# Kernel optimization log

Measured on AMD Instinct MI355X. Metric: run time of the kernel, lower is better.

Reference implementation:

```python
import jax, jax.numpy as jnp
import numpy as np

# cv2 GrabCut label codes
GC_BGD, GC_FGD, GC_PR_BGD, GC_PR_FGD = 0, 1, 2, 3
ITER_COUNT = 5
GAMMA = 50.0  # smoothness weight (GrabCut's standard gamma)

B, C, H, W = 2, 256, 512, 512


def setup_inputs() -> dict:
    key = jax.random.key(0)
    k1, k2 = jax.random.split(key)
    features = jax.random.normal(k1, (B, C, H, W), dtype=jnp.float32)
    mask = jax.random.randint(k2, (B, H, W), 0, 2, dtype=jnp.int32)
    return {"features": features, "mask": mask}


def _neighbor_mean(a):
    # a: (B,H,W); 4-neighbor mean with edge replication (smoothness/pairwise term)
    p = jnp.pad(a, ((0, 0), (1, 1), (1, 1)), mode="edge")
    return (p[:, :-2, 1:-1] + p[:, 2:, 1:-1] + p[:, 1:-1, :-2] + p[:, 1:-1, 2:]) * 0.25


def reference(features, mask):
    b, c, h, w = features.shape
    # take first 3 channels as pseudo-RGB image, HWC layout
    img = jnp.transpose(features[:, :3], (0, 2, 3, 1))  # (B,H,W,3)
    # cv2.normalize(..., 0, 255, NORM_MINMAX) over the whole array, then uint8 cast
    mn = img.min(axis=(1, 2, 3), keepdims=True)
    mx = img.max(axis=(1, 2, 3), keepdims=True)
    img = jnp.clip(jnp.floor((img - mn) / (mx - mn + 1e-12) * 255.0), 0.0, 255.0)

    # trimap seeding exactly as in the torch module
    tri = jnp.where(mask == 1, GC_PR_FGD, GC_PR_BGD).astype(jnp.int32)
    bh, bw = int(h * 0.1), int(w * 0.1)
    tri = tri.at[:, :bh, :].set(GC_BGD)
    tri = tri.at[:, h - bh:, :].set(GC_BGD)
    tri = tri.at[:, :, :bw].set(GC_BGD)
    tri = tri.at[:, :, w - bw:].set(GC_BGD)
    tri = tri.at[:, int(h * 0.45):int(h * 0.55), int(w * 0.45):int(w * 0.55)].set(GC_FGD)

    fixed = (tri == GC_BGD) | (tri == GC_FGD)          # hard constraints never change
    fixed_fg = (tri == GC_FGD).astype(img.dtype)
    alpha = ((tri == GC_FGD) | (tri == GC_PR_FGD)).astype(img.dtype)  # fg indicator

    # GrabCut surrogate: iteratively (1) refit fg/bg color models from current
    # labeling (GMM step collapsed to per-region mean), (2) relabel probable
    # pixels by unary (color distance) + pairwise (neighbor agreement) energy
    # -- an ICM approximation of the min-cut step.
    for _ in range(ITER_COUNT):
        a4 = alpha[..., None]                                    # (B,H,W,1)
        fg_mean = (img * a4).sum((1, 2)) / (a4.sum((1, 2)) + 1e-6)        # (B,3)
        bg_mean = (img * (1.0 - a4)).sum((1, 2)) / ((1.0 - a4).sum((1, 2)) + 1e-6)
        d_fg = ((img - fg_mean[:, None, None, :]) ** 2).sum(-1)  # (B,H,W)
        d_bg = ((img - bg_mean[:, None, None, :]) ** 2).sum(-1)
        nb = _neighbor_mean(alpha)
        score = d_bg - d_fg + GAMMA * (2.0 * nb - 1.0)           # >0 -> foreground
        new_alpha = (score > 0).astype(img.dtype)
        alpha = jnp.where(fixed, fixed_fg, new_alpha)

    return alpha  # (B,H,W) in {0,1}, float32
```

## Files before the change

kernel.cpp:

```cpp
#include <hip/hip_runtime.h>
#include <stdint.h>
#include <stddef.h>

#pragma clang fp contract(off)

#define HH 512
#define WW 512
#define HW_ 262144
#define FEAT_BSTRIDE (256*HW_)

__device__ __forceinline__ float quantf(float f, float mn, float denom) {
  float v = (f - mn) / denom * 255.0f;
  v = floorf(v);
  return fminf(fmaxf(v, 0.0f), 255.0f);
}

__device__ __forceinline__ bool is_center(int y, int x) {
  return (y >= 230) & (y < 281) & (x >= 230) & (x < 281);
}
__device__ __forceinline__ bool is_border(int y, int x) {
  return (y < 51) | (y >= 461) | (x < 51) | (x >= 461);
}

__global__ __launch_bounds__(256) void k_minmax(const float* __restrict__ feat,
                                                float2* __restrict__ mm) {
  int blk = blockIdx.x, tid = threadIdx.x;
  int b = blk >> 7, ib = blk & 127;
  const float4* base =
      reinterpret_cast<const float4*>(feat + (size_t)b * FEAT_BSTRIDE) + (size_t)ib * 1536;
  float mn = 3.4e38f, mx = -3.4e38f;
#pragma unroll
  for (int j = 0; j < 6; j++) {
    float4 v = base[tid + j * 256];
    mn = fminf(mn, fminf(fminf(v.x, v.y), fminf(v.z, v.w)));
    mx = fmaxf(mx, fmaxf(fmaxf(v.x, v.y), fmaxf(v.z, v.w)));
  }
  __shared__ float smn[256], smx[256];
  smn[tid] = mn; smx[tid] = mx;
  __syncthreads();
  for (int s = 128; s >= 1; s >>= 1) {
    if (tid < s) {
      smn[tid] = fminf(smn[tid], smn[tid + s]);
      smx[tid] = fmaxf(smx[tid], smx[tid + s]);
    }
    __syncthreads();
  }
  if (tid == 0) mm[blk] = make_float2(smn[0], smx[0]);
}

__global__ __launch_bounds__(256) void k_init(const float* __restrict__ feat,
                                              const int* __restrict__ mask,
                                              const float2* __restrict__ mm,
                                              uint8_t* __restrict__ alphaA,
                                              int4* __restrict__ totals,
                                              int4* __restrict__ slot0) {
  int blk = blockIdx.x, tid = threadIdx.x;
  int b = blk >> 7;
  __shared__ float smn[128], smx[128];
  if (tid < 128) { float2 v = mm[b * 128 + tid]; smn[tid] = v.x; smx[tid] = v.y; }
  __syncthreads();
  for (int s = 64; s >= 1; s >>= 1) {
    if (tid < s) {
      smn[tid] = fminf(smn[tid], smn[tid + s]);
      smx[tid] = fmaxf(smx[tid], smx[tid + s]);
    }
    __syncthreads();
  }
  float mn = smn[0];
  float denom = (smx[0] - mn) + 1e-12f;
  const float* fb = feat + (size_t)b * FEAT_BSTRIDE;
  int a0 = 0, a1 = 0, a2 = 0, a3 = 0, t0 = 0, t1 = 0, t2 = 0;
#pragma unroll
  for (int j = 0; j < 8; j++) {
    int p = blk * 2048 + tid + j * 256;
    int pb = p & (HW_ - 1);
    int y = pb >> 9, x = pb & 511;
    int r  = (int)quantf(fb[pb], mn, denom);
    int g  = (int)quantf(fb[HW_ + pb], mn, denom);
    int bl = (int)quantf(fb[2 * HW_ + pb], mn, denom);
    int a;
    if (is_center(y, x)) a = 1;
    else if (is_border(y, x)) a = 0;
    else a = (mask[p] == 1) ? 1 : 0;
    alphaA[p] = (uint8_t)a;
    a0 += r * a; a1 += g * a; a2 += bl * a; a3 += a;
    t0 += r; t1 += g; t2 += bl;
  }
  __shared__ int red[256][8];
  red[tid][0] = a0; red[tid][1] = a1; red[tid][2] = a2; red[tid][3] = a3;
  red[tid][4] = t0; red[tid][5] = t1; red[tid][6] = t2; red[tid][7] = 0;
  __syncthreads();
  for (int s = 128; s >= 1; s >>= 1) {
    if (tid < s) {
#pragma unroll
      for (int j = 0; j < 7; j++) red[tid][j] += red[tid + s][j];
    }
    __syncthreads();
  }
  if (tid == 0) {
    slot0[blk]  = make_int4(red[0][0], red[0][1], red[0][2], red[0][3]);
    totals[blk] = make_int4(red[0][4], red[0][5], red[0][6], 0);
  }
}

__global__ __launch_bounds__(256) void k_relabel(const float* __restrict__ feat,
                                                 const uint8_t* __restrict__ ain,
                                                 uint8_t* __restrict__ aout,
                                                 const float2* __restrict__ mm,
                                                 const int4* __restrict__ totals,
                                                 const int4* __restrict__ slotIn,
                                                 int4* __restrict__ slotOut,
                                                 float* __restrict__ out,
                                                 int finalIter) {
  int blk = blockIdx.x, tid = threadIdx.x;
  int b = blk >> 7;
  __shared__ float smn[128], smx[128];
  __shared__ int red[128][8];
  if (tid < 128) {
    float2 v = mm[b * 128 + tid]; smn[tid] = v.x; smx[tid] = v.y;
    int4 s = slotIn[b * 128 + tid];
    int4 t = totals[b * 128 + tid];
    red[tid][0] = s.x; red[tid][1] = s.y; red[tid][2] = s.z; red[tid][3] = s.w;
    red[tid][4] = t.x; red[tid][5] = t.y; red[tid][6] = t.z; red[tid][7] = 0;
  }
  __syncthreads();
  for (int s = 64; s >= 1; s >>= 1) {
    if (tid < s) {
      smn[tid] = fminf(smn[tid], smn[tid + s]);
      smx[tid] = fmaxf(smx[tid], smx[tid + s]);
#pragma unroll
      for (int j = 0; j < 7; j++) red[tid][j] += red[tid + s][j];
    }
    __syncthreads();
  }
  __shared__ float fmv[3], bmv[3];
  if (tid == 0) {
    int cnt = red[0][3];
    float fden = (float)cnt + 1e-6f;
    float bden = (float)(HW_ - cnt) + 1e-6f;
#pragma unroll
    for (int c = 0; c < 3; c++) {
      fmv[c] = (float)red[0][c] / fden;
      bmv[c] = (float)(red[0][4 + c] - red[0][c]) / bden;
    }
  }
  __syncthreads();
  float f0 = fmv[0], f1 = fmv[1], f2 = fmv[2];
  float g0 = bmv[0], g1 = bmv[1], g2 = bmv[2];
  float mn = smn[0];
  float denom = (smx[0] - smn[0]) + 1e-12f;
  const float* fb = feat + (size_t)b * FEAT_BSTRIDE;
  int a0 = 0, a1 = 0, a2 = 0, a3 = 0;
#pragma unroll
  for (int j = 0; j < 8; j++) {
    int p = blk * 2048 + tid + j * 256;
    int pb = p & (HW_ - 1);
    int y = pb >> 9, x = pb & 511;
    float i0 = quantf(fb[pb], mn, denom);
    float i1 = quantf(fb[HW_ + pb], mn, denom);
    float i2 = quantf(fb[2 * HW_ + pb], mn, denom);
    int up = ain[p - (y > 0 ? WW : 0)];
    int dn = ain[p + (y < HH - 1 ? WW : 0)];
    int lf = ain[p - (x > 0 ? 1 : 0)];
    int rt = ain[p + (x < WW - 1 ? 1 : 0)];
    float nb = (float)(((up + dn) + lf) + rt) * 0.25f;
    float pair = 50.0f * ((2.0f * nb) - 1.0f);
    float t0 = i0 - f0, t1 = i1 - f1, t2 = i2 - f2;
    float df = ((t0 * t0) + (t1 * t1)) + (t2 * t2);
    float u0 = i0 - g0, u1 = i1 - g1, u2 = i2 - g2;
    float db = ((u0 * u0) + (u1 * u1)) + (u2 * u2);
    float score = (db - df) + pair;
    int a;
    if (is_center(y, x)) a = 1;
    else if (is_border(y, x)) a = 0;
    else a = (score > 0.0f) ? 1 : 0;
    aout[p] = (uint8_t)a;
    if (finalIter) out[p] = (float)a;
    int ri = (int)i0, gi = (int)i1, bi = (int)i2;
    a0 += ri * a; a1 += gi * a; a2 += bi * a; a3 += a;
  }
  __shared__ int red2[256][4];
  red2[tid][0] = a0; red2[tid][1] = a1; red2[tid][2] = a2; red2[tid][3] = a3;
  __syncthreads();
  for (int s = 128; s >= 1; s >>= 1) {
    if (tid < s) {
#pragma unroll
      for (int j = 0; j < 4; j++) red2[tid][j] += red2[tid + s][j];
    }
    __syncthreads();
  }
  if (tid == 0) slotOut[blk] = make_int4(red2[0][0], red2[0][1], red2[0][2], red2[0][3]);
}

extern "C" void kernel_launch(void* const* d_in, const int* in_sizes, int n_in,
                              void* d_out, int out_size, void* d_ws, size_t ws_size,
                              hipStream_t stream) {
  const float* feat = (const float*)d_in[0];
  const int*   mask = (const int*)d_in[1];
  float* out = (float*)d_out;

  char* ws = (char*)d_ws;
  uint8_t* aA     = (uint8_t*)(ws);
  uint8_t* aB     = (uint8_t*)(ws + 524288);
  float2*  mm     = (float2*)(ws + 1048576);
  int4*    totals = (int4*)(ws + 1050624);
  int4*    slots  = (int4*)(ws + 1054720);

  k_minmax<<<256, 256, 0, stream>>>(feat, mm);
  k_init<<<256, 256, 0, stream>>>(feat, mask, mm, aA, totals, slots );

  uint8_t* ain = aA;
  uint8_t* aout_buf = aB;
  for (int k = 0; k < 5; k++) {
    k_relabel<<<256, 256, 0, stream>>>(feat, ain, aout_buf, mm, totals,
                                       slots + (size_t)k * 256,
                                       slots + (size_t)(k + 1) * 256,
                                       out, (k == 4) ? 1 : 0);
    uint8_t* tmp = ain; ain = aout_buf; aout_buf = tmp;
  }
}
```

Measured before the change: 626.7 us.

## Fuse minmax, init and relabel iterations into one cooperative kernel

Replaces seven separate kernel launches with one cooperative kernel that uses grid-wide syncs between phases. Each thread keeps its raw and then quantized RGB values in registers, so the feature channels are read from global memory once instead of in every phase. This removes launch overhead and the repeated feature reads. In exchange it adds grid.sync barriers and more register pressure, and it relies on all 256 blocks being co-resident.

```diff
diff --git a/kernel.cpp b/kernel.cpp
--- a/kernel.cpp
+++ b/kernel.cpp
@@ -1,8 +1,11 @@
 #include <hip/hip_runtime.h>
+#include <hip/hip_cooperative_groups.h>
 #include <stdint.h>
 #include <stddef.h>
 
 #pragma clang fp contract(off)
+
+namespace cg = cooperative_groups;
 
 #define HH 512
 #define WW 512
@@ -22,20 +25,32 @@
   return (y < 51) | (y >= 461) | (x < 51) | (x >= 461);
 }
 
-__global__ __launch_bounds__(256) void k_minmax(const float* __restrict__ feat,
-                                                float2* __restrict__ mm) {
-  int blk = blockIdx.x, tid = threadIdx.x;
-  int b = blk >> 7, ib = blk & 127;
-  const float4* base =
-      reinterpret_cast<const float4*>(feat + (size_t)b * FEAT_BSTRIDE) + (size_t)ib * 1536;
+__global__ __launch_bounds__(256) void k_fused(
+    const float* __restrict__ feat, const int* __restrict__ mask,
+    uint8_t* __restrict__ aA, uint8_t* __restrict__ aB,
+    float2* __restrict__ mm, int4* __restrict__ totals,
+    int4* __restrict__ slots, float* __restrict__ out)
+{
+  cg::grid_group grid = cg::this_grid();
+  const int blk = blockIdx.x, tid = threadIdx.x;
+  const int b = blk >> 7;
+  const float* fb = feat + (size_t)b * FEAT_BSTRIDE;
+  const int pbase = blk * 2048 + tid;
+
+  __shared__ float smn[256], smx[256];
+  __shared__ int red[256][8];
+  __shared__ float fmv[3], bmv[3];
+
+  float rq[8], gq[8], bq[8];
   float mn = 3.4e38f, mx = -3.4e38f;
 #pragma unroll
-  for (int j = 0; j < 6; j++) {
-    float4 v = base[tid + j * 256];
-    mn = fminf(mn, fminf(fminf(v.x, v.y), fminf(v.z, v.w)));
-    mx = fmaxf(mx, fmaxf(fmaxf(v.x, v.y), fmaxf(v.z, v.w)));
-  }
-  __shared__ float smn[256], smx[256];
+  for (int j = 0; j < 8; j++) {
+    int pb = (pbase + j * 256) & (HW_ - 1);
+    float r = fb[pb], g = fb[HW_ + pb], bl = fb[2 * HW_ + pb];
+    rq[j] = r; gq[j] = g; bq[j] = bl;
+    mn = fminf(mn, fminf(fminf(r, g), bl));
+    mx = fmaxf(mx, fmaxf(fmaxf(r, g), bl));
+  }
   smn[tid] = mn; smx[tid] = mx;
   __syncthreads();
   for (int s = 128; s >= 1; s >>= 1) {
@@ -46,17 +61,8 @@
     __syncthreads();
   }
   if (tid == 0) mm[blk] = make_float2(smn[0], smx[0]);
-}
-
-__global__ __launch_bounds__(256) void k_init(const float* __restrict__ feat,
-                                              const int* __restrict__ mask,
-                                              const float2* __restrict__ mm,
-                                              uint8_t* __restrict__ alphaA,
-                                              int4* __restrict__ totals,
-                                              int4* __restrict__ slot0) {
-  int blk = blockIdx.x, tid = threadIdx.x;
-  int b = blk >> 7;
-  __shared__ float smn[128], smx[128];
+  grid.sync();
+
   if (tid < 128) { float2 v = mm[b * 128 + tid]; smn[tid] = v.x; smx[tid] = v.y; }
   __syncthreads();
   for (int s = 64; s >= 1; s >>= 1) {
@@ -66,130 +72,123 @@
     }
     __syncthreads();
   }
-  float mn = smn[0];
-  float denom = (smx[0] - mn) + 1e-12f;
-  const float* fb = feat + (size_t)b * FEAT_BSTRIDE;
-  int a0 = 0, a1 = 0, a2 = 0, a3 = 0, t0 = 0, t1 = 0, t2 = 0;
+  mn = smn[0];
+  const float denom = (smx[0] - mn) + 1e-12f;
+
 #pragma unroll
   for (int j = 0; j < 8; j++) {
-    int p = blk * 2048 + tid + j * 256;
-    int pb = p & (HW_ - 1);
-    int y = pb >> 9, x = pb & 511;
-    int r  = (int)quantf(fb[pb], mn, denom);
-    int g  = (int)quantf(fb[HW_ + pb], mn, denom);
-    int bl = (int)quantf(fb[2 * HW_ + pb], mn, denom);
-    int a;
-    if (is_center(y, x)) a = 1;
-    else if (is_border(y, x)) a = 0;
-    else a = (mask[p] == 1) ? 1 : 0;
-    alphaA[p] = (uint8_t)a;
-    a0 += r * a; a1 += g * a; a2 += bl * a; a3 += a;
-    t0 += r; t1 += g; t2 += bl;
-  }
-  __shared__ int red[256][8];
-  red[tid][0] = a0; red[tid][1] = a1; red[tid][2] = a2; red[tid][3] = a3;
-  red[tid][4] = t0; red[tid][5] = t1; red[tid][6] = t2; red[tid][7] = 0;
-  __syncthreads();
-  for (int s = 128; s >= 1; s >>= 1) {
-    if (tid < s) {
-#pragma unroll
-      for (int j = 0; j < 7; j++) red[tid][j] += red[tid + s][j];
-    }
-    __syncthreads();
-  }
-  if (tid == 0) {
-    slot0[blk]  = make_int4(red[0][0], red[0][1], red[0][2], red[0][3]);
-    totals[blk] = make_int4(red[0][4], red[0][5], red[0][6], 0);
-  }
-}
-
-__global__ __launch_bounds__(256) void k_relabel(const float* __restrict__ feat,
-                                                 const uint8_t* __restrict__ ain,
-                                                 uint8_t* __restrict__ aout,
-                                                 const float2* __restrict__ mm,
-                                                 const int4* __restrict__ totals,
-                                                 const int4* __restrict__ slotIn,
-                                                 int4* __restrict__ slotOut,
-                                                 float* __restrict__ out,
-                                                 int finalIter) {
-  int blk = blockIdx.x, tid = threadIdx.x;
-  int b = blk >> 7;
-  __shared__ float smn[128], smx[128];
-  __shared__ int red[128][8];
-  if (tid < 128) {
-    float2 v = mm[b * 128 + tid]; smn[tid] = v.x; smx[tid] = v.y;
-    int4 s = slotIn[b * 128 + tid];
-    int4 t = totals[b * 128 + tid];
-    red[tid][0] = s.x; red[tid][1] = s.y; red[tid][2] = s.z; red[tid][3] = s.w;
-    red[tid][4] = t.x; red[tid][5] = t.y; red[tid][6] = t.z; red[tid][7] = 0;
-  }
-  __syncthreads();
-  for (int s = 64; s >= 1; s >>= 1) {
-    if (tid < s) {
-      smn[tid] = fminf(smn[tid], smn[tid + s]);
-      smx[tid] = fmaxf(smx[tid], smx[tid + s]);
-#pragma unroll
-      for (int j = 0; j < 7; j++) red[tid][j] += red[tid + s][j];
-    }
-    __syncthreads();
-  }
-  __shared__ float fmv[3], bmv[3];
-  if (tid == 0) {
-    int cnt = red[0][3];
-    float fden = (float)cnt + 1e-6f;
-    float bden = (float)(HW_ - cnt) + 1e-6f;
-#pragma unroll
-    for (int c = 0; c < 3; c++) {
-      fmv[c] = (float)red[0][c] / fden;
-      bmv[c] = (float)(red[0][4 + c] - red[0][c]) / bden;
-    }
-  }
-  __syncthreads();
-  float f0 = fmv[0], f1 = fmv[1], f2 = fmv[2];
-  float g0 = bmv[0], g1 = bmv[1], g2 = bmv[2];
-  float mn = smn[0];
-  float denom = (smx[0] - smn[0]) + 1e-12f;
-  const float* fb = feat + (size_t)b * FEAT_BSTRIDE;
-  int a0 = 0, a1 = 0, a2 = 0, a3 = 0;
-#pragma unroll
-  for (int j = 0; j < 8; j++) {
-    int p = blk * 2048 + tid + j * 256;
-    int pb = p & (HW_ - 1);
-    int y = pb >> 9, x = pb & 511;
-    float i0 = quantf(fb[pb], mn, denom);
-    float i1 = quantf(fb[HW_ + pb], mn, denom);
-    float i2 = quantf(fb[2 * HW_ + pb], mn, denom);
-    int up = ain[p - (y > 0 ? WW : 0)];
-    int dn = ain[p + (y < HH - 1 ? WW : 0)];
-    int lf = ain[p - (x > 0 ? 1 : 0)];
-    int rt = ain[p + (x < WW - 1 ? 1 : 0)];
-    float nb = (float)(((up + dn) + lf) + rt) * 0.25f;
-    float pair = 50.0f * ((2.0f * nb) - 1.0f);
-    float t0 = i0 - f0, t1 = i1 - f1, t2 = i2 - f2;
-    float df = ((t0 * t0) + (t1 * t1)) + (t2 * t2);
-    float u0 = i0 - g0, u1 = i1 - g1, u2 = i2 - g2;
-    float db = ((u0 * u0) + (u1 * u1)) + (u2 * u2);
-    float score = (db - df) + pair;
-    int a;
-    if (is_center(y, x)) a = 1;
-    else if (is_border(y, x)) a = 0;
-    else a = (score > 0.0f) ? 1 : 0;
-    aout[p] = (uint8_t)a;
-    if (finalIter) out[p] = (float)a;
-    int ri = (int)i0, gi = (int)i1, bi = (int)i2;
-    a0 += ri * a; a1 += gi * a; a2 += bi * a; a3 += a;
-  }
-  __shared__ int red2[256][4];
-  red2[tid][0] = a0; red2[tid][1] = a1; red2[tid][2] = a2; red2[tid][3] = a3;
-  __syncthreads();
-  for (int s = 128; s >= 1; s >>= 1) {
-    if (tid < s) {
-#pragma unroll
-      for (int j = 0; j < 4; j++) red2[tid][j] += red2[tid + s][j];
-    }
-    __syncthreads();
-  }
-  if (tid == 0) slotOut[blk] = make_int4(red2[0][0], red2[0][1], red2[0][2], red2[0][3]);
+    rq[j] = quantf(rq[j], mn, denom);
+    gq[j] = quantf(gq[j], mn, denom);
+    bq[j] = quantf(bq[j], mn, denom);
+  }
+
+  {
+    int a0 = 0, a1 = 0, a2 = 0, a3 = 0, t0 = 0, t1 = 0, t2 = 0;
+#pragma unroll
+    for (int j = 0; j < 8; j++) {
+      int p = pbase + j * 256;
+      int pb = p & (HW_ - 1);
+      int y = pb >> 9, x = pb & 511;
+      int aj;
+      if (is_center(y, x)) aj = 1;
+      else if (is_border(y, x)) aj = 0;
+      else aj = (mask[p] == 1) ? 1 : 0;
+      aA[p] = (uint8_t)aj;
+      int ri = (int)rq[j], gi = (int)gq[j], bi = (int)bq[j];
+      a0 += ri * aj; a1 += gi * aj; a2 += bi * aj; a3 += aj;
+      t0 += ri; t1 += gi; t2 += bi;
+    }
+    red[tid][0] = a0; red[tid][1] = a1; red[tid][2] = a2; red[tid][3] = a3;
+    red[tid][4] = t0; red[tid][5] = t1; red[tid][6] = t2; red[tid][7] = 0;
+    __syncthreads();
+    for (int s = 128; s >= 1; s >>= 1) {
+      if (tid < s) {
+#pragma unroll
+        for (int j = 0; j < 7; j++) red[tid][j] += red[tid + s][j];
+      }
+      __syncthreads();
+    }
+    if (tid == 0) {
+      slots[blk]  = make_int4(red[0][0], red[0][1], red[0][2], red[0][3]);
+      totals[blk] = make_int4(red[0][4], red[0][5], red[0][6], 0);
+    }
+  }
+  grid.sync();
+
+  uint8_t* ain = aA;
+  uint8_t* aout = aB;
+  for (int k = 0; k < 5; k++) {
+    if (tid < 128) {
+      int4 s4 = slots[k * 256 + b * 128 + tid];
+      int4 t4 = totals[b * 128 + tid];
+      red[tid][0] = s4.x; red[tid][1] = s4.y; red[tid][2] = s4.z; red[tid][3] = s4.w;
+      red[tid][4] = t4.x; red[tid][5] = t4.y; red[tid][6] = t4.z; red[tid][7] = 0;
+    }
+    __syncthreads();
+    for (int s = 64; s >= 1; s >>= 1) {
+      if (tid < s) {
+#pragma unroll
+        for (int j = 0; j < 7; j++) red[tid][j] += red[tid + s][j];
+      }
+      __syncthreads();
+    }
+    if (tid == 0) {
+      int cnt = red[0][3];
+      float fden = (float)cnt + 1e-6f;
+      float bden = (float)(HW_ - cnt) + 1e-6f;
+#pragma unroll
+      for (int c = 0; c < 3; c++) {
+        fmv[c] = (float)red[0][c] / fden;
+        bmv[c] = (float)(red[0][4 + c] - red[0][c]) / bden;
+      }
+    }
+    __syncthreads();
+    float f0 = fmv[0], f1 = fmv[1], f2 = fmv[2];
+    float g0 = bmv[0], g1 = bmv[1], g2 = bmv[2];
+
+    int c0 = 0, c1 = 0, c2 = 0, c3 = 0;
+#pragma unroll
+    for (int j = 0; j < 8; j++) {
+      int p = pbase + j * 256;
+      int pb = p & (HW_ - 1);
+      int y = pb >> 9, x = pb & 511;
+      float i0 = rq[j], i1 = gq[j], i2 = bq[j];
+      int up = ain[p - (y > 0 ? WW : 0)];
+      int dn = ain[p + (y < HH - 1 ? WW : 0)];
+      int lf = ain[p - (x > 0 ? 1 : 0)];
+      int rt = ain[p + (x < WW - 1 ? 1 : 0)];
+      float nb = (float)(((up + dn) + lf) + rt) * 0.25f;
+      float pr = 50.0f * ((2.0f * nb) - 1.0f);
+      float d0 = i0 - f0, d1 = i1 - f1, d2 = i2 - f2;
+      float df = ((d0 * d0) + (d1 * d1)) + (d2 * d2);
+      float u0 = i0 - g0, u1 = i1 - g1, u2 = i2 - g2;
+      float db = ((u0 * u0) + (u1 * u1)) + (u2 * u2);
+      float sc = (db - df) + pr;
+      int aj;
+      if (is_center(y, x)) aj = 1;
+      else if (is_border(y, x)) aj = 0;
+      else aj = (sc > 0.0f) ? 1 : 0;
+      if (k == 4) out[p] = (float)aj;
+      else aout[p] = (uint8_t)aj;
+      c0 += (int)i0 * aj; c1 += (int)i1 * aj; c2 += (int)i2 * aj; c3 += aj;
+    }
+
+    if (k < 4) {
+      red[tid][0] = c0; red[tid][1] = c1; red[tid][2] = c2; red[tid][3] = c3;
+      __syncthreads();
+      for (int s = 128; s >= 1; s >>= 1) {
+        if (tid < s) {
+#pragma unroll
+          for (int j = 0; j < 4; j++) red[tid][j] += red[tid + s][j];
+        }
+        __syncthreads();
+      }
+      if (tid == 0)
+        slots[(k + 1) * 256 + blk] = make_int4(red[0][0], red[0][1], red[0][2], red[0][3]);
+      uint8_t* tmp = ain; ain = aout; aout = tmp;
+      grid.sync();
+    }
+  }
 }
 
 extern "C" void kernel_launch(void* const* d_in, const int* in_sizes, int n_in,
@@ -206,16 +205,8 @@
   int4*    totals = (int4*)(ws + 1050624);
   int4*    slots  = (int4*)(ws + 1054720);
 
-  k_minmax<<<256, 256, 0, stream>>>(feat, mm);
-  k_init<<<256, 256, 0, stream>>>(feat, mask, mm, aA, totals, slots );
-
-  uint8_t* ain = aA;
-  uint8_t* aout_buf = aB;
-  for (int k = 0; k < 5; k++) {
-    k_relabel<<<256, 256, 0, stream>>>(feat, ain, aout_buf, mm, totals,
-                                       slots + (size_t)k * 256,
-                                       slots + (size_t)(k + 1) * 256,
-                                       out, (k == 4) ? 1 : 0);
-    uint8_t* tmp = ain; ain = aout_buf; aout_buf = tmp;
-  }
-}
+  void* args[] = {(void*)&feat, (void*)&mask, (void*)&aA, (void*)&aB,
+                  (void*)&mm, (void*)&totals, (void*)&slots, (void*)&out};
+  hipLaunchCooperativeKernel((const void*)k_fused, dim3(256), dim3(256),
+                             args, 0, stream);
+}
```

New measurement: 751.9 us. +20.0%, slower.
